# Kernel tuning notes

Hardware: AMD Instinct MI355X
Metric: run time of the kernel (lower is better)

The kernel has to match this reference:

```python
import jax, jax.numpy as jnp
import numpy as np

B, S, HID = 1, 2048, 4096
N_HEADS, N_KV_HEADS = 32, 8
HEAD_DIM = HID // N_HEADS  # 128


def setup_inputs() -> dict:
    key = jax.random.key(0)
    ks = jax.random.split(key, 5)
    w = 0.02  # init scale for weights
    return {
        "hidden_states": jax.random.normal(ks[0], (B, S, HID), dtype=jnp.float32),
        "Wq": jax.random.normal(ks[1], (HID, HID), dtype=jnp.float32) * w,
        "Wk": jax.random.normal(ks[2], (N_KV_HEADS * HEAD_DIM, HID), dtype=jnp.float32) * w,
        "Wv": jax.random.normal(ks[3], (N_KV_HEADS * HEAD_DIM, HID), dtype=jnp.float32) * w,
        "Wo": jax.random.normal(ks[4], (HID, HID), dtype=jnp.float32) * w,
        "n_init": 4,
        "n_local": 1024,
    }


def reference(hidden_states, Wq, Wk, Wv, Wo, n_init, n_local):
    b, s, hid = hidden_states.shape
    n_rep = N_HEADS // N_KV_HEADS
    scale = 1.0 / np.sqrt(HEAD_DIM).astype(np.float32)

    # QKV projections (torch Linear: y = x @ W.T)
    q = (hidden_states @ Wq.T).reshape(b, s, N_HEADS, HEAD_DIM).transpose(0, 2, 1, 3)
    k = (hidden_states @ Wk.T).reshape(b, s, N_KV_HEADS, HEAD_DIM).transpose(0, 2, 1, 3)
    v = (hidden_states @ Wv.T).reshape(b, s, N_KV_HEADS, HEAD_DIM).transpose(0, 2, 1, 3)

    # GQA: repeat KV heads to match query heads
    k = jnp.repeat(k, n_rep, axis=1)  # [b, H, s, d]
    v = jnp.repeat(v, n_rep, axis=1)

    scores = jnp.einsum('bhqd,bhkd->bhqk', q, k) * scale  # [b, H, s, s]

    # StreamingLLM mask: causal AND (attention sink OR sliding window)
    i = jnp.arange(s)[:, None]
    j = jnp.arange(s)[None, :]
    allowed = (j <= i) & ((j < n_init) | (i - j < n_local))  # [s, s]
    neg = jnp.finfo(scores.dtype).min
    scores = jnp.where(allowed[None, None], scores, neg)

    probs = jax.nn.softmax(scores, axis=-1)
    attn = jnp.einsum('bhqk,bhkd->bhqd', probs, v)  # [b, H, s, d]
    attn = attn.transpose(0, 2, 1, 3).reshape(b, s, hid)
    return attn @ Wo.T
```

## Files before the change

### kernel.cpp

```cpp
#include <hip/hip_runtime.h>
#include <hip/hip_bf16.h>

#define S     2048
#define HID   4096
#define NH    32
#define NKV   8
#define DH    128
#define KVD   1024
#define NQK   6144
#define KDIM  4096

typedef unsigned short ushort_t;
typedef __attribute__((ext_vector_type(8))) __bf16 bf16x8;
typedef __attribute__((ext_vector_type(8))) unsigned short u16x8;
typedef __attribute__((ext_vector_type(4))) float f32x4;

static __device__ __forceinline__ unsigned short f2b(float f) {
    union { float f; unsigned int i; } x; x.f = f;
    unsigned int r = (x.i + 0x7fffu + ((x.i >> 16) & 1u)) >> 16;
    return (unsigned short)r;
}

static __device__ __forceinline__ void gload16(const void* g, void* l) {
    __builtin_amdgcn_global_load_lds(
        (const __attribute__((address_space(1))) void*)g,
        (__attribute__((address_space(3))) void*)l, 16, 0, 0);
}

__global__ __launch_bounds__(256)
void cvt_f2b(const float* __restrict__ src, ushort_t* __restrict__ dst, int n4) {
    int i = blockIdx.x * 256 + threadIdx.x;
    if (i < n4) {
        float4 v = ((const float4*)src)[i];
        ushort4 o;
        o.x = f2b(v.x); o.y = f2b(v.y); o.z = f2b(v.z); o.w = f2b(v.w);
        ((ushort4*)dst)[i] = o;
    }
}

#define G_BM 256
#define G_BN 128
#define G_BK 64
#define BUF_USH ((G_BM + G_BN) * G_BK)
#define BOFF_B  (G_BM * G_BK)

#define STG_A(bb, kt2, j) gload16(gA[j] + (size_t)(kt2) * G_BK, &sm[(bb) + ldA[j]])
#define STG_B(bb, kt2, j) gload16(gB[j] + (size_t)(kt2) * G_BK, &sm[(bb) + ldB[j]])

template <int MODE>
__global__ __launch_bounds__(512, 2)
void gemm256(const ushort_t* __restrict__ A, const ushort_t* __restrict__ B,
             float* __restrict__ Cf, ushort_t* __restrict__ Qb,
             ushort_t* __restrict__ Kb, ushort_t* __restrict__ Vt,
             int M, int N, int K) {
    __shared__ __align__(16) ushort_t sm[3 * BUF_USH];

    const int tid   = threadIdx.x;
    const int w     = tid >> 6;
    const int lane  = tid & 63;
    const int mlane = lane & 15;
    const int q4    = lane >> 4;
    const int wr    = w >> 1, wc = w & 1;
    const int m0    = blockIdx.y * G_BM;
    const int n0    = blockIdx.x * G_BN;

    const ushort_t* gA[4];
    const ushort_t* gB[2];
    int ldA[4], ldB[2];
#pragma unroll
    for (int j = 0; j < 4; j++) {
        int c = j * 512 + tid, row = c >> 3, sl = (c & 7) ^ (row & 7);
        gA[j]  = A + (size_t)(m0 + row) * K + sl * 8;
        ldA[j] = (j * 512 + w * 64) * 8;
    }
#pragma unroll
    for (int j = 0; j < 2; j++) {
        int c = j * 512 + tid, row = c >> 3, sl = (c & 7) ^ (row & 7);
        gB[j]  = B + (size_t)(n0 + row) * K + sl * 8;
        ldB[j] = BOFF_B + (j * 512 + w * 64) * 8;
    }

    int offA[4][2], offB[4][2];
#pragma unroll
    for (int f = 0; f < 4; f++)
#pragma unroll
        for (int ks = 0; ks < 2; ks++) {
            int ra = wr * 64 + f * 16 + mlane;
            offA[f][ks] = ra * 64 + (((ks * 4 + q4) ^ (ra & 7)) * 8);
            int rb = wc * 64 + f * 16 + mlane;
            offB[f][ks] = BOFF_B + rb * 64 + (((ks * 4 + q4) ^ (rb & 7)) * 8);
        }

    f32x4 acc[4][4];
#pragma unroll
    for (int i = 0; i < 4; i++)
#pragma unroll
        for (int j = 0; j < 4; j++) acc[i][j] = (f32x4)(0.0f);

    const int NT = K / G_BK;

    STG_A(0, 0, 0); STG_A(0, 0, 1); STG_A(0, 0, 2); STG_A(0, 0, 3);
    STG_B(0, 0, 0); STG_B(0, 0, 1);
    STG_A(BUF_USH, 1, 0); STG_A(BUF_USH, 1, 1);
    STG_A(BUF_USH, 1, 2); STG_A(BUF_USH, 1, 3);
    STG_B(BUF_USH, 1, 0); STG_B(BUF_USH, 1, 1);
    asm volatile("s_waitcnt vmcnt(6)" ::: "memory");
    __builtin_amdgcn_s_barrier();

    int s_cur = 0;
    for (int kt = 0; kt < NT; kt++) {
        const int s_n2 = (s_cur >= 1) ? s_cur - 1 : 2;
        const int base = s_cur * BUF_USH;
        const int b2   = s_n2 * BUF_USH;
        const bool stg = (kt + 2) < NT;

#pragma unroll
        for (int p = 0; p < 2; p++) {
            bf16x8 af2[4], bq2[4];
#pragma unroll
            for (int f = 0; f < 4; f++)
                af2[f] = *(const bf16x8*)&sm[base + offA[f][p]];
#pragma unroll
            for (int f = 0; f < 4; f++)
                bq2[f] = *(const bf16x8*)&sm[base + offB[f][p]];

            if (stg) {
                if (p == 0) { STG_A(b2, kt + 2, 0); STG_A(b2, kt + 2, 1);
                              STG_B(b2, kt + 2, 0); }
                else        { STG_A(b2, kt + 2, 2); STG_A(b2, kt + 2, 3);
                              STG_B(b2, kt + 2, 1); }
            }

            __builtin_amdgcn_s_barrier();
            asm volatile("s_waitcnt lgkmcnt(0)");
            __builtin_amdgcn_s_setprio(1);
#pragma unroll
            for (int mt = 0; mt < 4; mt++)
#pragma unroll
                for (int nt = 0; nt < 4; nt++)
                    acc[mt][nt] = __builtin_amdgcn_mfma_f32_16x16x32_bf16(
                        af2[mt], bq2[nt], acc[mt][nt], 0, 0, 0);
            __builtin_amdgcn_s_setprio(0);
            __builtin_amdgcn_s_barrier();
        }

        if (stg) asm volatile("s_waitcnt vmcnt(6)" ::: "memory");
        else     asm volatile("s_waitcnt vmcnt(0)" ::: "memory");
        __builtin_amdgcn_s_barrier();
        s_cur = (s_cur == 2) ? 0 : s_cur + 1;
    }

#pragma unroll
    for (int fm = 0; fm < 4; fm++) {
#pragma unroll
        for (int fn = 0; fn < 4; fn++) {
            const int row = m0 + wr * 64 + fm * 16 + q4 * 4;
            const int col = n0 + wc * 64 + fn * 16 + mlane;
            if (MODE == 0) {
#pragma unroll
                for (int r = 0; r < 4; r++)
                    Cf[(size_t)(row + r) * N + col] = acc[fm][fn][r];
            } else {
                if (n0 < HID) {
#pragma unroll
                    for (int r = 0; r < 4; r++)
                        Qb[(size_t)(row + r) * HID + col] = f2b(acc[fm][fn][r]);
                } else if (n0 < HID + KVD) {
                    int c2 = col - HID;
#pragma unroll
                    for (int r = 0; r < 4; r++)
                        Kb[(size_t)(row + r) * KVD + c2] = f2b(acc[fm][fn][r]);
                } else {
                    int c2 = col - (HID + KVD);
                    ushort4 o;
                    o.x = f2b(acc[fm][fn][0]); o.y = f2b(acc[fm][fn][1]);
                    o.z = f2b(acc[fm][fn][2]); o.w = f2b(acc[fm][fn][3]);
                    *(ushort4*)(Vt + (size_t)c2 * S + row) = o;
                }
            }
        }
    }
}

__global__ __launch_bounds__(256)
void attn_mfma(const ushort_t* __restrict__ Qb, const ushort_t* __restrict__ Kb,
               const ushort_t* __restrict__ Vt, ushort_t* __restrict__ O,
               const int* __restrict__ n_init_p, const int* __restrict__ n_local_p) {
    __shared__ ushort_t Ks[4][32][40];
    __shared__ ushort_t Vs[128][40];
    __shared__ ushort_t Ps[4][16][40];

    const int n_init = *n_init_p, n_local = *n_local_p;
    const int tid   = threadIdx.x;
    const int w     = tid >> 6;
    const int lane  = tid & 63;
    const int mlane = lane & 15;
    const int q4    = lane >> 4;
    const int h     = blockIdx.x >> 5;
    const int qt    = blockIdx.x & 31;
    const int kh    = h >> 2;
    const int i0    = qt * 64;
    const int iMax  = i0 + 63;
    const int qrow_base = i0 + w * 16;

    bf16x8 qf[4];
    {
        const ushort_t* qp = Qb + (size_t)(qrow_base + mlane) * HID + h * DH + q4 * 8;
#pragma unroll
        for (int ks = 0; ks < 4; ks++) qf[ks] = *(const bf16x8*)(qp + ks * 32);
    }

    f32x4 oacc[8];
#pragma unroll
    for (int i = 0; i < 8; i++) oacc[i] = (f32x4)(0.0f);
    float lrow[4];
#pragma unroll
    for (int r = 0; r < 4; r++) lrow[r] = 0.0f;

    int wstart = i0 - n_local + 1; if (wstart < 0) wstart = 0;
    const int tw   = (wstart <= n_init) ? 0 : (wstart >> 5);
    const int tmax = iMax >> 5;
    const float scale = 0.08838834764831845f;

    const int skk = tid >> 4, sc = tid & 15;
    const int vd  = tid >> 2, vc = tid & 3;
    ushort_t* psw = &Ps[w][0][0];

    for (int t = 0; t <= tmax; t++) {
        if (t > 0 && t < tw) continue;
        const int j0 = t * 32;

        u16x8 ka = *(const u16x8*)(Kb + (size_t)(j0 + skk) * KVD + kh * DH + sc * 8);
        u16x8 kc = *(const u16x8*)(Kb + (size_t)(j0 + skk + 16) * KVD + kh * DH + sc * 8);
        u16x8 va = *(const u16x8*)(Vt + (size_t)(kh * DH + vd) * S + j0 + vc * 8);
        u16x8 vb = *(const u16x8*)(Vt + (size_t)(kh * DH + vd + 64) * S + j0 + vc * 8);
        __syncthreads();
        *(u16x8*)&Ks[sc >> 2][skk][(sc & 3) * 8] = ka;
        *(u16x8*)&Ks[sc >> 2][skk + 16][(sc & 3) * 8] = kc;
        *(u16x8*)&Vs[vd][vc * 8] = va;
        *(u16x8*)&Vs[vd + 64][vc * 8] = vb;
        __syncthreads();

        f32x4 sacc0 = (f32x4)(0.0f), sacc1 = (f32x4)(0.0f);
#pragma unroll
        for (int ks = 0; ks < 4; ks++) {
            bf16x8 k0f = *(const bf16x8*)&Ks[ks][mlane][q4 * 8];
            bf16x8 k1f = *(const bf16x8*)&Ks[ks][16 + mlane][q4 * 8];
            sacc0 = __builtin_amdgcn_mfma_f32_16x16x32_bf16(qf[ks], k0f, sacc0, 0, 0, 0);
            sacc1 = __builtin_amdgcn_mfma_f32_16x16x32_bf16(qf[ks], k1f, sacc1, 0, 0, 0);
        }

        const bool interior = (j0 + 31 <= i0) && (iMax - j0 < n_local);

#pragma unroll
        for (int r = 0; r < 4; r++) {
            float p0, p1;
            if (interior) {
                p0 = __expf(sacc0[r] * scale);
                p1 = __expf(sacc1[r] * scale);
            } else {
                int qi = qrow_base + q4 * 4 + r;
                int jA = j0 + mlane, jB = jA + 16;
                bool okA = (jA <= qi) && ((jA < n_init) || (qi - jA < n_local));
                bool okB = (jB <= qi) && ((jB < n_init) || (qi - jB < n_local));
                p0 = okA ? __expf(sacc0[r] * scale) : 0.0f;
                p1 = okB ? __expf(sacc1[r] * scale) : 0.0f;
            }
            lrow[r] += p0 + p1;
            psw[(q4 * 4 + r) * 40 + mlane]      = f2b(p0);
            psw[(q4 * 4 + r) * 40 + 16 + mlane] = f2b(p1);
        }

        bf16x8 pf = *(const bf16x8*)&psw[mlane * 40 + q4 * 8];
#pragma unroll
        for (int dt = 0; dt < 8; dt++) {
            bf16x8 vf = *(const bf16x8*)&Vs[dt * 16 + mlane][q4 * 8];
            oacc[dt] = __builtin_amdgcn_mfma_f32_16x16x32_bf16(pf, vf, oacc[dt], 0, 0, 0);
        }
    }

#pragma unroll
    for (int r = 0; r < 4; r++) {
#pragma unroll
        for (int off = 1; off < 16; off <<= 1)
            lrow[r] += __shfl_xor(lrow[r], off);
    }

#pragma unroll
    for (int r = 0; r < 4; r++) {
        float inv = 1.0f / lrow[r];
        int qrow = qrow_base + q4 * 4 + r;
        ushort_t* op = O + (size_t)qrow * HID + h * DH + mlane;
#pragma unroll
        for (int dt = 0; dt < 8; dt++)
            op[dt * 16] = f2b(oacc[dt][r] * inv);
    }
}

extern "C" void kernel_launch(void* const* d_in, const int* in_sizes, int n_in,
                              void* d_out, int out_size, void* d_ws, size_t ws_size,
                              hipStream_t stream) {
    const float* H  = (const float*)d_in[0];
    const float* Wq = (const float*)d_in[1];
    const float* Wk = (const float*)d_in[2];
    const float* Wv = (const float*)d_in[3];
    const float* Wo = (const float*)d_in[4];
    const int* n_init_p  = (const int*)d_in[5];
    const int* n_local_p = (const int*)d_in[6];

    char* p = (char*)d_ws;
    ushort_t* Hb   = (ushort_t*)p;  p += (size_t)S * HID * 2;
    ushort_t* Wbuf = (ushort_t*)p;  p += (size_t)NQK * KDIM * 2;
    ushort_t* Qb   = (ushort_t*)p;  p += (size_t)S * HID * 2;
    ushort_t* Kb   = (ushort_t*)p;  p += (size_t)S * KVD * 2;
    ushort_t* Vt   = (ushort_t*)p;
    ushort_t* Ab   = Hb;

    dim3 blk(256);
    const int nH = S * HID / 4, nWq = HID * KDIM / 4, nWk = KVD * KDIM / 4;

    cvt_f2b<<<dim3((nH  + 255) / 256), blk, 0, stream>>>(H,  Hb, nH);
    cvt_f2b<<<dim3((nWq + 255) / 256), blk, 0, stream>>>(Wq, Wbuf, nWq);
    cvt_f2b<<<dim3((nWk + 255) / 256), blk, 0, stream>>>(Wk, Wbuf + (size_t)HID * KDIM, nWk);
    cvt_f2b<<<dim3((nWk + 255) / 256), blk, 0, stream>>>(Wv, Wbuf + (size_t)(HID + KVD) * KDIM, nWk);
    gemm256<1><<<dim3(NQK / G_BN, S / G_BM), dim3(512), 0, stream>>>(
        Hb, Wbuf, nullptr, Qb, Kb, Vt, S, NQK, KDIM);
    attn_mfma<<<dim3(NH * (S / 64)), blk, 0, stream>>>(Qb, Kb, Vt, Ab, n_init_p, n_local_p);
    cvt_f2b<<<dim3((nWq + 255) / 256), blk, 0, stream>>>(Wo, Wbuf, nWq);
    gemm256<0><<<dim3(HID / G_BN, S / G_BM), dim3(512), 0, stream>>>(
        Ab, Wbuf, (float*)d_out, nullptr, nullptr, nullptr, S, HID, KDIM);
}
```

Before: 475.2 us.

## Software-pipeline LDS fragment loads against MFMA in GEMM main loop

```diff
diff --git a/kernel.cpp b/kernel.cpp
--- a/kernel.cpp
+++ b/kernel.cpp
@@ -107,47 +107,59 @@
     asm volatile("s_waitcnt vmcnt(6)" ::: "memory");
     __builtin_amdgcn_s_barrier();
 
+    bf16x8 afc[4], bqc[4], afn[4], bqn[4];
+#pragma unroll
+    for (int f = 0; f < 4; f++) {
+        afc[f] = *(const bf16x8*)&sm[offA[f][0]];
+        bqc[f] = *(const bf16x8*)&sm[offB[f][0]];
+    }
+
     int s_cur = 0;
     for (int kt = 0; kt < NT; kt++) {
-        const int s_n2 = (s_cur >= 1) ? s_cur - 1 : 2;
+        const int s_n1 = (s_cur == 2) ? 0 : s_cur + 1;
+        const int s_n2 = (s_n1  == 2) ? 0 : s_n1  + 1;
         const int base = s_cur * BUF_USH;
+        const int b1   = s_n1 * BUF_USH;
         const int b2   = s_n2 * BUF_USH;
         const bool stg = (kt + 2) < NT;
 
 #pragma unroll
-        for (int p = 0; p < 2; p++) {
-            bf16x8 af2[4], bq2[4];
-#pragma unroll
-            for (int f = 0; f < 4; f++)
-                af2[f] = *(const bf16x8*)&sm[base + offA[f][p]];
-#pragma unroll
-            for (int f = 0; f < 4; f++)
-                bq2[f] = *(const bf16x8*)&sm[base + offB[f][p]];
-
-            if (stg) {
-                if (p == 0) { STG_A(b2, kt + 2, 0); STG_A(b2, kt + 2, 1);
-                              STG_B(b2, kt + 2, 0); }
-                else        { STG_A(b2, kt + 2, 2); STG_A(b2, kt + 2, 3);
-                              STG_B(b2, kt + 2, 1); }
-            }
-
-            __builtin_amdgcn_s_barrier();
-            asm volatile("s_waitcnt lgkmcnt(0)");
-            __builtin_amdgcn_s_setprio(1);
-#pragma unroll
-            for (int mt = 0; mt < 4; mt++)
-#pragma unroll
-                for (int nt = 0; nt < 4; nt++)
-                    acc[mt][nt] = __builtin_amdgcn_mfma_f32_16x16x32_bf16(
-                        af2[mt], bq2[nt], acc[mt][nt], 0, 0, 0);
-            __builtin_amdgcn_s_setprio(0);
-            __builtin_amdgcn_s_barrier();
-        }
-
-        if (stg) asm volatile("s_waitcnt vmcnt(6)" ::: "memory");
+        for (int f = 0; f < 4; f++) {
+            afn[f] = *(const bf16x8*)&sm[base + offA[f][1]];
+            bqn[f] = *(const bf16x8*)&sm[base + offB[f][1]];
+        }
+        if (stg) { STG_A(b2, kt + 2, 0); STG_A(b2, kt + 2, 1); STG_B(b2, kt + 2, 0); }
+        __builtin_amdgcn_sched_barrier(0);
+        __builtin_amdgcn_s_setprio(1);
+#pragma unroll
+        for (int mt = 0; mt < 4; mt++)
+#pragma unroll
+            for (int nt = 0; nt < 4; nt++)
+                acc[mt][nt] = __builtin_amdgcn_mfma_f32_16x16x32_bf16(
+                    afc[mt], bqc[nt], acc[mt][nt], 0, 0, 0);
+        __builtin_amdgcn_s_setprio(0);
+        if (stg) asm volatile("s_waitcnt vmcnt(3)" ::: "memory");
         else     asm volatile("s_waitcnt vmcnt(0)" ::: "memory");
         __builtin_amdgcn_s_barrier();
-        s_cur = (s_cur == 2) ? 0 : s_cur + 1;
+
+#pragma unroll
+        for (int f = 0; f < 4; f++) {
+            afc[f] = *(const bf16x8*)&sm[b1 + offA[f][0]];
+            bqc[f] = *(const bf16x8*)&sm[b1 + offB[f][0]];
+        }
+        if (stg) { STG_A(b2, kt + 2, 2); STG_A(b2, kt + 2, 3); STG_B(b2, kt + 2, 1); }
+        __builtin_amdgcn_sched_barrier(0);
+        __builtin_amdgcn_s_setprio(1);
+#pragma unroll
+        for (int mt = 0; mt < 4; mt++)
+#pragma unroll
+            for (int nt = 0; nt < 4; nt++)
+                acc[mt][nt] = __builtin_amdgcn_mfma_f32_16x16x32_bf16(
+                    afn[mt], bqn[nt], acc[mt][nt], 0, 0, 0);
+        __builtin_amdgcn_s_setprio(0);
+        __builtin_amdgcn_s_barrier();
+        __builtin_amdgcn_sched_barrier(0);
+        s_cur = s_n1;
     }
 
 #pragma unroll
```

Result: no change. 466.3 us (-1.9%).
